# Performance work log

Measured on AMD Instinct MI355X. Metric: run time of the kernel, lower is better.

## Reference

```python
import jax, jax.numpy as jnp
from jax import lax
import numpy as np

B, N = 8, 16384
C = 16            # layer_channels
K = 2             # kernel_size
L = 30            # layer_nums (layer 0 is plain causal conv, 29 gated layers)
AGG = 64          # agregate1x1 out channels
OUT = 256         # output1x1 out channels (8-bit classes)


def causal_conv(x, w, dilation):
    # x: (B, Cin, N), w: (Cout, Cin, K) -> (B, Cout, N), left-padded (causal)
    k = w.shape[-1]
    return lax.conv_general_dilated(
        x, w, window_strides=(1,), padding=[(dilation * (k - 1), 0)],
        rhs_dilation=(dilation,), dimension_numbers=('NCH', 'OIH', 'NCH'))


def setup_inputs() -> dict:
    key = jax.random.key(0)
    ks = jax.random.split(key, 16)
    s = 0.1
    x = jax.random.normal(ks[0], (B, N), dtype=jnp.float32) * 8000.0  # raw 16-bit-ish audio
    lengths = jax.random.randint(ks[1], (B,), N // 2, N, dtype=jnp.int32)
    return {
        'x': x,
        'lengths': lengths,
        'W0': jax.random.normal(ks[2], (C, 1, K), dtype=jnp.float32) * s,
        'b0': jnp.zeros((C,), dtype=jnp.float32),
        'Wf': jax.random.normal(ks[3], (L - 1, C, C, K), dtype=jnp.float32) * s,
        'bf': jnp.zeros((L - 1, C), dtype=jnp.float32),
        'Wg': jax.random.normal(ks[4], (L - 1, C, C, K), dtype=jnp.float32) * s,
        'bg': jnp.zeros((L - 1, C), dtype=jnp.float32),
        'Wr': jax.random.normal(ks[5], (L - 1, C, C), dtype=jnp.float32) * s,
        'br': jnp.zeros((L - 1, C), dtype=jnp.float32),
        'Wa': jax.random.normal(ks[6], (AGG, C), dtype=jnp.float32) * s,
        'ba': jnp.zeros((AGG,), dtype=jnp.float32),
        'Wo': jax.random.normal(ks[7], (OUT, AGG), dtype=jnp.float32) * s,
        'bo': jnp.zeros((OUT,), dtype=jnp.float32),
    }


def reference(x, lengths, W0, b0, Wf, bf, Wg, bg, Wr, br, Wa, ba, Wo, bo):
    inp = (x / 32768.0)[:, None, :]                     # (B,1,N), 65536/2 scaling
    # layer 0: plain causal conv 1 -> C
    h = causal_conv(inp, W0, 1) + b0[:, None]           # (B,C,N)
    skip = h
    inp = inp + h                                       # (B,1,N)+(B,C,N) broadcast
    for i in range(1, L):
        d = 2 ** (i % 10)
        j = i - 1
        f = jnp.tanh(causal_conv(inp, Wf[j], d) + bf[j][:, None])
        g = jax.nn.sigmoid(causal_conv(inp, Wg[j], d) + bg[j][:, None])
        z = f * g                                       # gated activation
        out = jnp.einsum('oc,bcn->bon', Wr[j], z) + br[j][:, None]
        skip = skip + out                               # skip-sum accumulation
        inp = inp + out                                 # residual
    a = jnp.einsum('oc,bcn->bon', Wa, jax.nn.relu(skip)) + ba[:, None]
    o = jnp.einsum('oc,bcn->bon', Wo, jax.nn.relu(a)) + bo[:, None]
    logp = jax.nn.log_softmax(o, axis=1)                # (B,OUT,N)
    mask = (jnp.arange(N) < lengths[:, None])[:, None, :].astype(logp.dtype)
    return logp * mask
```

## Files before the change

### kernel.cpp

```cpp
#include <hip/hip_runtime.h>
#include <hip/hip_bf16.h>

#define NN 16384
#define NC 16
#define NPOSTOT 131072
#define NLAY 29
#define TOUT 256
#define LSTR 24

typedef float4 f4;
typedef short bf16x8 __attribute__((ext_vector_type(8)));
typedef float f32x4 __attribute__((ext_vector_type(4)));

#define OFF_WF 0
#define OFF_WG (NLAY * 512)
#define OFF_WR (2 * NLAY * 512)
#define OFF_WA (3 * NLAY * 512)
#define OFF_WO (3 * NLAY * 512 + 2048)
#define PK_TOT (OFF_WO + 16384)

static __device__ __forceinline__ short to_bf16(float f) {
    __hip_bfloat16 h = __float2bfloat16(f);
    short s;
    __builtin_memcpy(&s, &h, 2);
    return s;
}
static __device__ __forceinline__ float from_bf16(short s) {
    unsigned int u = ((unsigned int)(unsigned short)s) << 16;
    float f;
    __builtin_memcpy(&f, &u, 4);
    return f;
}

__global__ __launch_bounds__(256) void prepack_k(
    const float* __restrict__ Wf, const float* __restrict__ Wg,
    const float* __restrict__ Wr, const float* __restrict__ Wa,
    const float* __restrict__ Wo, short* __restrict__ pk)
{
    const int i = blockIdx.x * 256 + threadIdx.x;
    if (i >= PK_TOT) return;
    float val;
    if (i < OFF_WG) {
        const int j = i >> 9, r = i & 511, l = r >> 3, j8 = r & 7;
        const int o = l & 15, h = l >> 4;
        const int k = h * 8 + j8, tap = k >> 4, c = k & 15;
        val = Wf[((j * 16 + o) * 16 + c) * 2 + tap];
    } else if (i < OFF_WA) {
        const int i2 = i - OFF_WG;
        if (i2 < NLAY * 512) {
            const int j = i2 >> 9, r = i2 & 511, l = r >> 3, j8 = r & 7;
            const int o = l & 15, h = l >> 4;
            const int k = h * 8 + j8, tap = k >> 4, c = k & 15;
            val = Wg[((j * 16 + o) * 16 + c) * 2 + tap];
        } else {
            const int i3 = i2 - NLAY * 512;
            const int j = i3 >> 9, r = i3 & 511, l = r >> 3, j8 = r & 7;
            const int o = l & 15, h = l >> 4;
            val = (j8 < 4) ? Wr[j * 256 + o * 16 + h * 4 + j8] : 0.0f;
        }
    } else if (i < OFF_WO) {
        const int i2 = i - OFF_WA;
        const int mt = i2 >> 9, r = i2 & 511, l = r >> 3, j8 = r & 7;
        const int og = mt * 16 + (l & 15), h = l >> 4;
        const int k = h * 8 + j8;
        val = (k < 16) ? Wa[og * 16 + k] : 0.0f;
    } else {
        const int i2 = i - OFF_WO;
        const int qt = i2 >> 10, hf = (i2 >> 9) & 1, r = i2 & 511;
        const int l = r >> 3, j8 = r & 7;
        const int q = qt * 16 + (l & 15), h = l >> 4;
        const int kg = hf * 32 + (j8 >> 2) * 16 + h * 4 + (j8 & 3);
        val = Wo[q * 64 + kg];
    }
    pk[i] = to_bf16(val);
}

static __device__ __forceinline__ f32x4 gated_core2(
    bf16x8 bx, bf16x8 af_, bf16x8 ag_, bf16x8 ar_,
    f32x4 cf, f32x4 cg, f32x4 cr)
{
    const f32x4 fp = __builtin_amdgcn_mfma_f32_16x16x32_bf16(af_, bx, cf, 0, 0, 0);
    const f32x4 gp = __builtin_amdgcn_mfma_f32_16x16x32_bf16(ag_, bx, cg, 0, 0, 0);

    bf16x8 bz;
#pragma unroll
    for (int r = 0; r < 4; ++r) {
        const float ef = __expf(2.0f * fminf(fp[r], 43.0f));
        const float eg = __expf(-gp[r]);
        const float den = fmaf(ef, eg, ef) + (eg + 1.0f);
        bz[r] = to_bf16((ef - 1.0f) * __builtin_amdgcn_rcpf(den));
        bz[r + 4] = 0;
    }
    return __builtin_amdgcn_mfma_f32_16x16x32_bf16(ar_, bz, cr, 0, 0, 0);
}

struct SegCfg { int d[8]; int nl; int jbase; int H; int l0; };

constexpr SegCfg CFGS[9] = {
    {{2, 4, 8, 16, 32, 64, 0, 0},  6, 0,  128, 1},
    {{128, 256, 0, 0, 0, 0, 0, 0}, 2, 6,  256, 0},
    {{512, 1, 2, 4, 8, 16, 32, 0}, 7, 8,  64,  0},
    {{64, 128, 0, 0, 0, 0, 0, 0},  2, 15, 128, 0},
    {{256, 0, 0, 0, 0, 0, 0, 0},   1, 17, 0,   0},
    {{512, 1, 2, 4, 8, 16, 32, 0}, 7, 18, 64,  0},
    {{64, 128, 0, 0, 0, 0, 0, 0},  2, 25, 128, 0},
    {{256, 0, 0, 0, 0, 0, 0, 0},   1, 27, 0,   0},
    {{512, 0, 0, 0, 0, 0, 0, 0},   1, 28, 0,   0},
};

template<int KI>
__global__ __launch_bounds__((TOUT + CFGS[KI].H) * 2)
void fused_t(const short* __restrict__ src, const float* __restrict__ x,
             const float* __restrict__ W0, const float* __restrict__ b0,
             short* __restrict__ dst, const short* __restrict__ pk,
             const float* __restrict__ bfA, const float* __restrict__ bgA,
             const float* __restrict__ brA)
{
    constexpr SegCfg cfg = CFGS[KI];
    constexpr int H = cfg.H;
    constexpr int Wp = TOUT + H;
    __shared__ short lds[2 * Wp * LSTR];
    short* ldsA = lds;
    short* ldsB = lds + Wp * LSTR;

    const int t = threadIdx.x, lane = t & 63, wv = t >> 6;
    const int h = lane >> 4, i16 = lane & 15;
    const int tap = h >> 1, c0 = (h & 1) * 8;
    const int pbase = blockIdx.x * TOUT;
    const int bb = pbase >> 14, n0 = pbase & (NN - 1);
    const float* xrow = x + (size_t)bb * NN;
    const short* srow = src + (size_t)bb * NN * NC;

    const int l0r = wv * 32 + i16;
    const int l1r = l0r + 16;
    const int nA = n0 - H + l0r;
    const int nB = nA + 16;

    f32x4 res0, res1;

    {
        constexpr int d = cfg.d[0];
        constexpr int j = cfg.jbase;
        const bf16x8 af = *(const bf16x8*)(pk + OFF_WF + j * 512 + lane * 8);
        const bf16x8 ag = *(const bf16x8*)(pk + OFF_WG + j * 512 + lane * 8);
        const bf16x8 ar = *(const bf16x8*)(pk + OFF_WR + j * 512 + lane * 8);
        const f4 v1 = *(const f4*)(bfA + j * 16 + h * 4);
        const f4 v2 = *(const f4*)(bgA + j * 16 + h * 4);
        const f4 v3 = *(const f4*)(brA + j * 16 + h * 4);
        const f32x4 cf = {v1.x, v1.y, v1.z, v1.w};
        const f32x4 cg = {v2.x, v2.y, v2.z, v2.w};
        const f32x4 cr = {v3.x, v3.y, v3.z, v3.w};

        auto tile0 = [&](int l, int n, f32x4& res) {
            const int ns = tap ? n : n - d;
            bf16x8 bx = {0, 0, 0, 0, 0, 0, 0, 0};
            if (cfg.l0) {
                if (ns >= 0) {
                    const float xs = xrow[ns] * (1.0f / 32768.0f);
                    const float xm = (ns >= 1) ? xrow[ns - 1] * (1.0f / 32768.0f) : 0.0f;
#pragma unroll
                    for (int q2 = 0; q2 < 8; ++q2) {
                        const int c = c0 + q2;
                        bx[q2] = to_bf16(xs + fmaf(W0[c * 2], xm,
                                          fmaf(W0[c * 2 + 1], xs, b0[c])));
                    }
                }
            } else {
                if (ns >= 0) bx = *(const bf16x8*)(srow + (size_t)ns * NC + c0);
            }
            const f32x4 o = gated_core2(bx, af, ag, ar, cf, cg, cr);

            float r0, r1, r2, r3;
            if (cfg.l0) {
                if (n >= 0) {
                    const float xs = xrow[n] * (1.0f / 32768.0f);
                    const float xm = (n >= 1) ? xrow[n - 1] * (1.0f / 32768.0f) : 0.0f;
                    const int c = h * 4;
                    r0 = xs + fmaf(W0[c * 2 + 0], xm, fmaf(W0[c * 2 + 1], xs, b0[c + 0]));
                    r1 = xs + fmaf(W0[c * 2 + 2], xm, fmaf(W0[c * 2 + 3], xs, b0[c + 1]));
                    r2 = xs + fmaf(W0[c * 2 + 4], xm, fmaf(W0[c * 2 + 5], xs, b0[c + 2]));
                    r3 = xs + fmaf(W0[c * 2 + 6], xm, fmaf(W0[c * 2 + 7], xs, b0[c + 3]));
                } else { r0 = r1 = r2 = r3 = 0.0f; }
            } else {
                if (n >= 0) {
                    const short4 ov = *(const short4*)(srow + (size_t)n * NC + h * 4);
                    r0 = from_bf16(ov.x); r1 = from_bf16(ov.y);
                    r2 = from_bf16(ov.z); r3 = from_bf16(ov.w);
                } else { r0 = r1 = r2 = r3 = 0.0f; }
            }
            res[0] = r0 + o[0]; res[1] = r1 + o[1];
            res[2] = r2 + o[2]; res[3] = r3 + o[3];
            *(short4*)(ldsA + l * LSTR + h * 4) =
                make_short4(to_bf16(res[0]), to_bf16(res[1]),
                            to_bf16(res[2]), to_bf16(res[3]));
        };
        tile0(l0r, nA, res0);
        tile0(l1r, nB, res1);
    }
    __syncthreads();

    int cur = 0;
#pragma unroll
    for (int s = 1; s < cfg.nl; ++s) {
        const int d = cfg.d[s];
        const int j = cfg.jbase + s;
        const bf16x8 af = *(const bf16x8*)(pk + OFF_WF + j * 512 + lane * 8);
        const bf16x8 ag = *(const bf16x8*)(pk + OFF_WG + j * 512 + lane * 8);
        const bf16x8 ar = *(const bf16x8*)(pk + OFF_WR + j * 512 + lane * 8);
        const f4 v1 = *(const f4*)(bfA + j * 16 + h * 4);
        const f4 v2 = *(const f4*)(bgA + j * 16 + h * 4);
        const f4 v3 = *(const f4*)(brA + j * 16 + h * 4);
        const f32x4 cf = {v1.x, v1.y, v1.z, v1.w};
        const f32x4 cg = {v2.x, v2.y, v2.z, v2.w};
        const f32x4 cr = {v3.x, v3.y, v3.z, v3.w};
        const short* rb = cur ? ldsB : ldsA;
        short* wb = cur ? ldsA : ldsB;

        auto tileL = [&](int l, int n, f32x4& res) {
            const int nt = tap ? n : n - d;
            int lt = tap ? l : l - d;
            if (lt < 0) lt = 0;
            bf16x8 bx = {0, 0, 0, 0, 0, 0, 0, 0};
            if (nt >= 0) bx = *(const bf16x8*)(rb + lt * LSTR + c0);
            const f32x4 o = gated_core2(bx, af, ag, ar, cf, cg, cr);
            res[0] += o[0]; res[1] += o[1]; res[2] += o[2]; res[3] += o[3];
            *(short4*)(wb + l * LSTR + h * 4) =
                make_short4(to_bf16(res[0]), to_bf16(res[1]),
                            to_bf16(res[2]), to_bf16(res[3]));
        };
        tileL(l0r, nA, res0);
        tileL(l1r, nB, res1);
        __syncthreads();
        cur ^= 1;
    }

    if (l0r >= H) {
        *(short4*)(dst + ((size_t)bb * NN + nA) * NC + h * 4) =
            make_short4(to_bf16(res0[0]), to_bf16(res0[1]),
                        to_bf16(res0[2]), to_bf16(res0[3]));
    }
    if (l1r >= H) {
        *(short4*)(dst + ((size_t)bb * NN + nB) * NC + h * 4) =
            make_short4(to_bf16(res1[0]), to_bf16(res1[1]),
                        to_bf16(res1[2]), to_bf16(res1[3]));
    }
}

__global__ __launch_bounds__(512, 2) void headm_k(
    const short* __restrict__ fin, const float* __restrict__ x,
    const int* __restrict__ lengths,
    const short* __restrict__ pka, const float* __restrict__ ba,
    const short* __restrict__ pko, const float* __restrict__ bo,
    float* __restrict__ out)
{
    __shared__ short ldsW[16384];

    const int t = threadIdx.x;
    const int lane = t & 63;
    const int wv = t >> 6;
    const int i16 = lane & 15;
    const int h = lane >> 4;
    const int pos = blockIdx.x * 128 + wv * 16 + i16;
    const int b = pos >> 14;
    const int n = pos & (NN - 1);

#pragma unroll
    for (int i = 0; i < 4; ++i)
        ((f4*)ldsW)[t + i * 512] = ((const f4*)pko)[t + i * 512];

    bf16x8 bs;
    if (h < 2) {
        const float xs = x[pos] * (1.0f / 32768.0f);
        const bf16x8 v = *(const bf16x8*)(fin + (size_t)pos * NC + h * 8);
#pragma unroll
        for (int j = 0; j < 8; ++j)
            bs[j] = to_bf16(fmaxf(from_bf16(v[j]) - xs, 0.0f));
    } else {
#pragma unroll
        for (int j = 0; j < 8; ++j) bs[j] = 0;
    }

    float ra[16];
#pragma unroll
    for (int mt = 0; mt < 4; ++mt) {
        const bf16x8 aa = *(const bf16x8*)(pka + (mt * 64 + lane) * 8);
        const f4 bav = *(const f4*)(ba + mt * 16 + h * 4);
        f32x4 c = {bav.x, bav.y, bav.z, bav.w};
        c = __builtin_amdgcn_mfma_f32_16x16x32_bf16(aa, bs, c, 0, 0, 0);
#pragma unroll
        for (int r = 0; r < 4; ++r) ra[mt * 4 + r] = fmaxf(c[r], 0.0f);
    }
    bf16x8 blo, bhi;
#pragma unroll
    for (int j = 0; j < 8; ++j) { blo[j] = to_bf16(ra[j]); bhi[j] = to_bf16(ra[8 + j]); }

    __syncthreads();

    float lg[64];
#pragma unroll
    for (int qt = 0; qt < 16; ++qt) {
        const bf16x8 a0 = *(const bf16x8*)(ldsW + ((qt * 2 + 0) * 64 + lane) * 8);
        const bf16x8 a1 = *(const bf16x8*)(ldsW + ((qt * 2 + 1) * 64 + lane) * 8);
        const f4 bov = *(const f4*)(bo + qt * 16 + h * 4);
        f32x4 c = {bov.x, bov.y, bov.z, bov.w};
        c = __builtin_amdgcn_mfma_f32_16x16x32_bf16(a0, blo, c, 0, 0, 0);
        c = __builtin_amdgcn_mfma_f32_16x16x32_bf16(a1, bhi, c, 0, 0, 0);
#pragma unroll
        for (int r = 0; r < 4; ++r) lg[qt * 4 + r] = c[r];
    }

    float m = lg[0];
#pragma unroll
    for (int j = 1; j < 64; ++j) m = fmaxf(m, lg[j]);
    m = fmaxf(m, __shfl_xor(m, 16, 64));
    m = fmaxf(m, __shfl_xor(m, 32, 64));
    float s = 0.0f;
#pragma unroll
    for (int j = 0; j < 64; ++j) s += __expf(lg[j] - m);
    s += __shfl_xor(s, 16, 64);
    s += __shfl_xor(s, 32, 64);
    const float lse = m + __logf(s);
    const bool valid = n < lengths[b];

    float* ob = out + (size_t)b * 256 * NN + n;
#pragma unroll
    for (int qt = 0; qt < 16; ++qt)
#pragma unroll
        for (int r = 0; r < 4; ++r)
            ob[(size_t)(qt * 16 + h * 4 + r) * NN] = valid ? (lg[qt * 4 + r] - lse) : 0.0f;
}

extern "C" void kernel_launch(void* const* d_in, const int* in_sizes, int n_in,
                              void* d_out, int out_size, void* d_ws, size_t ws_size,
                              hipStream_t stream)
{
    const float* x       = (const float*)d_in[0];
    const int*   lengths = (const int*)d_in[1];
    const float* W0      = (const float*)d_in[2];
    const float* b0      = (const float*)d_in[3];
    const float* Wf      = (const float*)d_in[4];
    const float* bf      = (const float*)d_in[5];
    const float* Wg      = (const float*)d_in[6];
    const float* bg      = (const float*)d_in[7];
    const float* Wr      = (const float*)d_in[8];
    const float* br      = (const float*)d_in[9];
    const float* Wa      = (const float*)d_in[10];
    const float* ba      = (const float*)d_in[11];
    const float* Wo      = (const float*)d_in[12];
    const float* bo      = (const float*)d_in[13];
    float* out = (float*)d_out;

    short* bufA = (short*)d_ws;
    short* bufB = bufA + (size_t)NPOSTOT * NC;
    short* pk   = bufB + (size_t)NPOSTOT * NC;

    prepack_k<<<dim3((PK_TOT + 255) / 256), dim3(256), 0, stream>>>(
        Wf, Wg, Wr, Wa, Wo, pk);

#define FUSED(K, SRC, DST)                                                     \
    fused_t<K><<<dim3(NPOSTOT / TOUT), dim3((TOUT + CFGS[K].H) * 2), 0,        \
                 stream>>>(SRC, x, W0, b0, DST, pk, bf, bg, br)

    FUSED(0, bufA, bufA);
    FUSED(1, bufA, bufB);
    FUSED(2, bufB, bufA);
    FUSED(3, bufA, bufB);
    FUSED(4, bufB, bufA);
    FUSED(5, bufA, bufB);
    FUSED(6, bufB, bufA);
    FUSED(7, bufA, bufB);
    FUSED(8, bufB, bufA);
#undef FUSED

    headm_k<<<dim3(NPOSTOT / 128), dim3(512), 0, stream>>>(
        bufA, x, lengths, pk + OFF_WA, ba, pk + OFF_WO, bo, out);
}
```

Before: 145.2 us.

## Use fixed 256-thread blocks with more tiles per wave and smaller output tiles

After: 151.2 us. +4.2%, slower.

```diff
diff --git a/kernel.cpp b/kernel.cpp
--- a/kernel.cpp
+++ b/kernel.cpp
@@ -5,7 +5,7 @@
 #define NC 16
 #define NPOSTOT 131072
 #define NLAY 29
-#define TOUT 256
+#define TOUT 128
 #define LSTR 24
 
 typedef float4 f4;
@@ -109,7 +109,7 @@
 };
 
 template<int KI>
-__global__ __launch_bounds__((TOUT + CFGS[KI].H) * 2)
+__global__ __launch_bounds__(256, ((TOUT + CFGS[KI].H) / 64 <= 4) ? 4 : 3)
 void fused_t(const short* __restrict__ src, const float* __restrict__ x,
              const float* __restrict__ W0, const float* __restrict__ b0,
              short* __restrict__ dst, const short* __restrict__ pk,
@@ -119,6 +119,7 @@
     constexpr SegCfg cfg = CFGS[KI];
     constexpr int H = cfg.H;
     constexpr int Wp = TOUT + H;
+    constexpr int T = Wp / 64;
     __shared__ short lds[2 * Wp * LSTR];
     short* ldsA = lds;
     short* ldsB = lds + Wp * LSTR;
@@ -131,12 +132,7 @@
     const float* xrow = x + (size_t)bb * NN;
     const short* srow = src + (size_t)bb * NN * NC;
 
-    const int l0r = wv * 32 + i16;
-    const int l1r = l0r + 16;
-    const int nA = n0 - H + l0r;
-    const int nB = nA + 16;
-
-    f32x4 res0, res1;
+    f32x4 res[T];
 
     {
         constexpr int d = cfg.d[0];
@@ -151,9 +147,15 @@
         const f32x4 cg = {v2.x, v2.y, v2.z, v2.w};
         const f32x4 cr = {v3.x, v3.y, v3.z, v3.w};
 
-        auto tile0 = [&](int l, int n, f32x4& res) {
+        bf16x8 bx[T];
+        f32x4 rin[T];
+#pragma unroll
+        for (int k = 0; k < T; ++k) {
+            const int l = (wv + 4 * k) * 16 + i16;
+            const int n = n0 - H + l;
             const int ns = tap ? n : n - d;
-            bf16x8 bx = {0, 0, 0, 0, 0, 0, 0, 0};
+            bf16x8 b = {0, 0, 0, 0, 0, 0, 0, 0};
+            f32x4 r = {0.0f, 0.0f, 0.0f, 0.0f};
             if (cfg.l0) {
                 if (ns >= 0) {
                     const float xs = xrow[ns] * (1.0f / 32768.0f);
@@ -161,41 +163,41 @@
 #pragma unroll
                     for (int q2 = 0; q2 < 8; ++q2) {
                         const int c = c0 + q2;
-                        bx[q2] = to_bf16(xs + fmaf(W0[c * 2], xm,
-                                          fmaf(W0[c * 2 + 1], xs, b0[c])));
+                        b[q2] = to_bf16(xs + fmaf(W0[c * 2], xm,
+                                         fmaf(W0[c * 2 + 1], xs, b0[c])));
                     }
                 }
-            } else {
-                if (ns >= 0) bx = *(const bf16x8*)(srow + (size_t)ns * NC + c0);
-            }
-            const f32x4 o = gated_core2(bx, af, ag, ar, cf, cg, cr);
-
-            float r0, r1, r2, r3;
-            if (cfg.l0) {
                 if (n >= 0) {
                     const float xs = xrow[n] * (1.0f / 32768.0f);
                     const float xm = (n >= 1) ? xrow[n - 1] * (1.0f / 32768.0f) : 0.0f;
                     const int c = h * 4;
-                    r0 = xs + fmaf(W0[c * 2 + 0], xm, fmaf(W0[c * 2 + 1], xs, b0[c + 0]));
-                    r1 = xs + fmaf(W0[c * 2 + 2], xm, fmaf(W0[c * 2 + 3], xs, b0[c + 1]));
-                    r2 = xs + fmaf(W0[c * 2 + 4], xm, fmaf(W0[c * 2 + 5], xs, b0[c + 2]));
-                    r3 = xs + fmaf(W0[c * 2 + 6], xm, fmaf(W0[c * 2 + 7], xs, b0[c + 3]));
-                } else { r0 = r1 = r2 = r3 = 0.0f; }
+                    r[0] = xs + fmaf(W0[c * 2 + 0], xm, fmaf(W0[c * 2 + 1], xs, b0[c + 0]));
+                    r[1] = xs + fmaf(W0[c * 2 + 2], xm, fmaf(W0[c * 2 + 3], xs, b0[c + 1]));
+                    r[2] = xs + fmaf(W0[c * 2 + 4], xm, fmaf(W0[c * 2 + 5], xs, b0[c + 2]));
+                    r[3] = xs + fmaf(W0[c * 2 + 6], xm, fmaf(W0[c * 2 + 7], xs, b0[c + 3]));
+                }
             } else {
+                if (ns >= 0) b = *(const bf16x8*)(srow + (size_t)ns * NC + c0);
                 if (n >= 0) {
                     const short4 ov = *(const short4*)(srow + (size_t)n * NC + h * 4);
-                    r0 = from_bf16(ov.x); r1 = from_bf16(ov.y);
-                    r2 = from_bf16(ov.z); r3 = from_bf16(ov.w);
-                } else { r0 = r1 = r2 = r3 = 0.0f; }
+                    r[0] = from_bf16(ov.x); r[1] = from_bf16(ov.y);
+                    r[2] = from_bf16(ov.z); r[3] = from_bf16(ov.w);
+                }
             }
-            res[0] = r0 + o[0]; res[1] = r1 + o[1];
-            res[2] = r2 + o[2]; res[3] = r3 + o[3];
-            *(short4*)(ldsA + l * LSTR + h * 4) =
-                make_short4(to_bf16(res[0]), to_bf16(res[1]),
-                            to_bf16(res[2]), to_bf16(res[3]));
-        };
-        tile0(l0r, nA, res0);
-        tile0(l1r, nB, res1);
+            bx[k] = b;
+            rin[k] = r;
+        }
+#pragma unroll
+        for (int k = 0; k < T; ++k) {
+            const f32x4 o = gated_core2(bx[k], af, ag, ar, cf, cg, cr);
+            res[k] = rin[k] + o;
+            if (cfg.nl > 1) {
+                const int l = (wv + 4 * k) * 16 + i16;
+                *(short4*)(ldsA + l * LSTR + h * 4) =
+                    make_short4(to_bf16(res[k][0]), to_bf16(res[k][1]),
+                                to_bf16(res[k][2]), to_bf16(res[k][3]));
+            }
+        }
     }
     __syncthreads();
 
@@ -216,33 +218,39 @@
         const short* rb = cur ? ldsB : ldsA;
         short* wb = cur ? ldsA : ldsB;
 
-        auto tileL = [&](int l, int n, f32x4& res) {
+        bf16x8 bx[T];
+#pragma unroll
+        for (int k = 0; k < T; ++k) {
+            const int l = (wv + 4 * k) * 16 + i16;
+            const int n = n0 - H + l;
             const int nt = tap ? n : n - d;
             int lt = tap ? l : l - d;
             if (lt < 0) lt = 0;
-            bf16x8 bx = {0, 0, 0, 0, 0, 0, 0, 0};
-            if (nt >= 0) bx = *(const bf16x8*)(rb + lt * LSTR + c0);
-            const f32x4 o = gated_core2(bx, af, ag, ar, cf, cg, cr);
-            res[0] += o[0]; res[1] += o[1]; res[2] += o[2]; res[3] += o[3];
+            bf16x8 b = {0, 0, 0, 0, 0, 0, 0, 0};
+            if (nt >= 0) b = *(const bf16x8*)(rb + lt * LSTR + c0);
+            bx[k] = b;
+        }
+#pragma unroll
+        for (int k = 0; k < T; ++k) {
+            const f32x4 o = gated_core2(bx[k], af, ag, ar, cf, cg, cr);
+            res[k] += o;
+            const int l = (wv + 4 * k) * 16 + i16;
             *(short4*)(wb + l * LSTR + h * 4) =
-                make_short4(to_bf16(res[0]), to_bf16(res[1]),
-                            to_bf16(res[2]), to_bf16(res[3]));
-        };
-        tileL(l0r, nA, res0);
-        tileL(l1r, nB, res1);
+                make_short4(to_bf16(res[k][0]), to_bf16(res[k][1]),
+                            to_bf16(res[k][2]), to_bf16(res[k][3]));
+        }
         __syncthreads();
         cur ^= 1;
     }
 
-    if (l0r >= H) {
-        *(short4*)(dst + ((size_t)bb * NN + nA) * NC + h * 4) =
-            make_short4(to_bf16(res0[0]), to_bf16(res0[1]),
-                        to_bf16(res0[2]), to_bf16(res0[3]));
-    }
-    if (l1r >= H) {
-        *(short4*)(dst + ((size_t)bb * NN + nB) * NC + h * 4) =
-            make_short4(to_bf16(res1[0]), to_bf16(res1[1]),
-                        to_bf16(res1[2]), to_bf16(res1[3]));
+#pragma unroll
+    for (int k = 0; k < T; ++k) {
+        const int l = (wv + 4 * k) * 16 + i16;
+        if (l < H) continue;
+        const int n = n0 - H + l;
+        *(short4*)(dst + ((size_t)bb * NN + n) * NC + h * 4) =
+            make_short4(to_bf16(res[k][0]), to_bf16(res[k][1]),
+                        to_bf16(res[k][2]), to_bf16(res[k][3]));
     }
 }
 
@@ -358,8 +366,8 @@
         Wf, Wg, Wr, Wa, Wo, pk);
 
 #define FUSED(K, SRC, DST)                                                     \
-    fused_t<K><<<dim3(NPOSTOT / TOUT), dim3((TOUT + CFGS[K].H) * 2), 0,        \
-                 stream>>>(SRC, x, W0, b0, DST, pk, bf, bg, br)
+    fused_t<K><<<dim3(NPOSTOT / TOUT), dim3(256), 0, stream>>>(                \
+        SRC, x, W0, b0, DST, pk, bf, bg, br)
 
     FUSED(0, bufA, bufA);
     FUSED(1, bufA, bufB);
```
